# Kernel tuning notes

Hardware: AMD Instinct MI355X
Metric: run time of the kernel (lower is better)

## Reference

```python
import jax, jax.numpy as jnp
import numpy as np

D_MODEL = 512
D_INNER = 1024   # expand * d_model
NH = 16          # heads (headdim 64)
HD = 64
NS = 16          # d_state
HID = 1024       # ff hidden = expand * d_model


def _ln(x, w, b, eps=1e-5):
    m = x.mean(-1, keepdims=True)
    v = ((x - m) ** 2).mean(-1, keepdims=True)
    return (x - m) * jax.lax.rsqrt(v + eps) * w + b


def _rms(x, w, eps=1e-5):
    return x * jax.lax.rsqrt((x * x).mean(-1, keepdims=True) + eps) * w


def _tree_scan(dt, xh, Bv, Cv, pidx, A):
    # dt:[B,T,W,H] xh:[B,T,W,H,P] Bv,Cv:[B,T,W,N] pidx:[B,T,W] A:[H]
    B_, T, W, H = dt.shape
    P = xh.shape[-1]
    N = Bv.shape[-1]
    h0 = jnp.zeros((B_, W, H, P, N), dt.dtype)
    xs = (jnp.moveaxis(dt, 1, 0), jnp.moveaxis(xh, 1, 0),
          jnp.moveaxis(Bv, 1, 0), jnp.moveaxis(Cv, 1, 0),
          jnp.moveaxis(pidx, 1, 0))

    def step(h, inp):
        dt_t, xh_t, b_t, c_t, p_t = inp
        # gather parent state from previous level along the width axis
        hp = jnp.take_along_axis(h, p_t[:, :, None, None, None], axis=1)  # [B,W,H,P,N]
        dA = jnp.exp(dt_t * A)                                            # [B,W,H]
        h_new = dA[..., None, None] * hp \
              + dt_t[..., None, None] * xh_t[..., None] * b_t[:, :, None, None, :]
        y_t = jnp.einsum('bwhpn,bwn->bwhp', h_new, c_t)
        return h_new, y_t

    _, ys = jax.lax.scan(step, h0, xs)
    return jnp.moveaxis(ys, 0, 1)  # [B,T,W,H,P]


def setup_inputs() -> dict:
    key = jax.random.key(0)
    ks = jax.random.split(key, 12)
    B, T, W = 8, 64, 16
    d_in_proj = 2 * D_INNER + 2 * NS + NH  # z | x | B | C | dt
    inp = {
        'x': jax.random.normal(ks[0], (B, T, W, D_MODEL), jnp.float32),
        'parent_pos': jax.random.randint(ks[1], (B, T, W), 0, W, dtype=jnp.int32),
        'ln1_w': jnp.ones((D_MODEL,), jnp.float32),
        'ln1_b': jnp.zeros((D_MODEL,), jnp.float32),
        'in_w': jax.random.normal(ks[2], (D_MODEL, d_in_proj), jnp.float32) * 0.02,
        'in_b': jnp.zeros((d_in_proj,), jnp.float32),
        'A_log': jnp.log(jax.random.uniform(ks[3], (NH,), jnp.float32, 1.0, 16.0)),
        'dt_bias': jnp.full((NH,), -4.0, jnp.float32),
        'Dp': jnp.ones((NH,), jnp.float32),
        'norm_w': jnp.ones((D_INNER,), jnp.float32),
        'out_w': jax.random.normal(ks[4], (D_INNER, D_MODEL), jnp.float32) * 0.02,
        'out_b': jnp.zeros((D_MODEL,), jnp.float32),
        'ln2_w': jnp.ones((D_MODEL,), jnp.float32),
        'ln2_b': jnp.zeros((D_MODEL,), jnp.float32),
        'ff1_w': jax.random.normal(ks[5], (D_MODEL, 2 * HID), jnp.float32) * 0.02,
        'ff1_b': jnp.zeros((2 * HID,), jnp.float32),
        'ff2_w': jax.random.normal(ks[6], (HID, D_MODEL), jnp.float32) * 0.02,
        'ff2_b': jnp.zeros((D_MODEL,), jnp.float32),
    }
    return inp


def reference(x, parent_pos, ln1_w, ln1_b, in_w, in_b, A_log, dt_bias, Dp,
              norm_w, out_w, out_b, ln2_w, ln2_b, ff1_w, ff1_b, ff2_w, ff2_b):
    # norm1 + TreeMamba2 + residual
    xn = _ln(x, ln1_w, ln1_b)
    proj = xn @ in_w + in_b
    z, xp, Bv, Cv, dtr = jnp.split(
        proj, [D_INNER, 2 * D_INNER, 2 * D_INNER + NS, 2 * D_INNER + 2 * NS], axis=-1)
    dt = jax.nn.softplus(dtr + dt_bias)            # [B,T,W,NH]
    A = -jnp.exp(A_log)                            # [NH]
    xh = xp.reshape(*xp.shape[:-1], NH, HD)        # [B,T,W,NH,HD]
    y = _tree_scan(dt, xh, Bv, Cv, parent_pos, A)  # [B,T,W,NH,HD]
    y = y + Dp[..., None] * xh                     # skip connection D*x
    y = y.reshape(*y.shape[:-2], D_INNER)
    y = _rms(y * jax.nn.silu(z), norm_w)           # gated RMSNorm
    y = y @ out_w + out_b
    x = y + x
    # norm2 + gated FF + residual
    yn = _ln(x, ln2_w, ln2_b)
    f = yn @ ff1_w + ff1_b
    f1, g = jnp.split(f, 2, axis=-1)
    f = (f1 * jax.nn.silu(g)) @ ff2_w + ff2_b
    return x + f
```

## Files before the change

### kernel.cpp

```cpp
#include <hip/hip_runtime.h>
#include <hip/hip_bf16.h>
#include <cmath>

#define D_MODEL 512
#define D_INNER 1024
#define NHEAD 16
#define HDIM 64
#define NSTATE 16
#define NB 8
#define NT 64
#define NW 16
#define MROWS 8192
#define PROJ_LD 2176
#define NPROJ 2096

typedef __attribute__((ext_vector_type(8))) short short8;
typedef __attribute__((ext_vector_type(4))) float f32x4;
typedef __hip_bfloat16 bf16;
typedef unsigned int u32;

__device__ __forceinline__ u32 fbits(float f) { return __float_as_uint(f); }
__device__ __forceinline__ float ubits(u32 u) { return __uint_as_float(u); }
__device__ __forceinline__ u32 pack_bf(float a, float b) {
  return (fbits(b) & 0xffff0000u) | (fbits(a) >> 16);
}

template<int N> __device__ __forceinline__ void vmwait() {
  if constexpr (N == 0)      asm volatile("s_waitcnt vmcnt(0)" ::: "memory");
  else if constexpr (N == 2) asm volatile("s_waitcnt vmcnt(2)" ::: "memory");
  else if constexpr (N == 3) asm volatile("s_waitcnt vmcnt(3)" ::: "memory");
  else if constexpr (N == 4) asm volatile("s_waitcnt vmcnt(4)" ::: "memory");
  else if constexpr (N == 6) asm volatile("s_waitcnt vmcnt(6)" ::: "memory");
  else if constexpr (N == 8) asm volatile("s_waitcnt vmcnt(8)" ::: "memory");
  else static_assert(N == 0, "unsupported vmcnt");
}

__device__ __forceinline__ float block_sum(float v, float* sbuf) {
#pragma unroll
  for (int o = 32; o > 0; o >>= 1) v += __shfl_down(v, o, 64);
  int lane = threadIdx.x & 63, wid = threadIdx.x >> 6;
  if (lane == 0) sbuf[wid] = v;
  __syncthreads();
  if (threadIdx.x == 0) {
    float t = 0.f;
    for (int i = 0; i < 4; i++) t += sbuf[i];
    sbuf[0] = t;
  }
  __syncthreads();
  return sbuf[0];
}

__global__ __launch_bounds__(256) void ln512_bf16_kernel(
    const float* __restrict__ x, const float* __restrict__ w,
    const float* __restrict__ b, bf16* __restrict__ out) {
  __shared__ float s1[8], s2[8];
  int row = blockIdx.x;
  const float* xr = x + (size_t)row * D_MODEL;
  bf16* outr = out + (size_t)row * D_MODEL;
  int c0 = threadIdx.x, c1 = threadIdx.x + 256;
  float v0 = xr[c0], v1 = xr[c1];
  float s  = block_sum(v0 + v1, s1);
  float ss = block_sum(v0 * v0 + v1 * v1, s2);
  float mean = s * (1.f / 512.f);
  float var  = ss * (1.f / 512.f) - mean * mean;
  float inv  = rsqrtf(var + 1e-5f);
  outr[c0] = __float2bfloat16((v0 - mean) * inv * w[c0] + b[c0]);
  outr[c1] = __float2bfloat16((v1 - mean) * inv * w[c1] + b[c1]);
}

__global__ __launch_bounds__(256) void wconv_all_kernel(
    const float* __restrict__ in_w, bf16* __restrict__ in_wt,
    const float* __restrict__ out_w, bf16* __restrict__ out_wt,
    const float* __restrict__ ff1_w, bf16* __restrict__ ff1_wt,
    const float* __restrict__ ff2_w, bf16* __restrict__ ff2_wt) {
  __shared__ float tile[32][33];
  int id = blockIdx.x;
  const float* w; bf16* wt;
  int K, N, Npad, bx, by;
  if (id < 1088)      { w = in_w;  wt = in_wt;  K = 512;  N = NPROJ; Npad = PROJ_LD; bx = id % 68;  by = id / 68; }
  else if (id < 1600) { int j = id - 1088; w = out_w; wt = out_wt; K = 1024; N = 512;  Npad = 512;  bx = j % 16; by = j / 16; }
  else if (id < 2624) { int j = id - 1600; w = ff1_w; wt = ff1_wt; K = 512;  N = 2048; Npad = 2048; bx = j % 64; by = j / 64; }
  else                { int j = id - 2624; w = ff2_w; wt = ff2_wt; K = 1024; N = 512;  Npad = 512;  bx = j % 16; by = j / 16; }
  int n0 = bx * 32, k0 = by * 32;
  int tx = threadIdx.x & 31, ty = threadIdx.x >> 5;
#pragma unroll
  for (int i = 0; i < 4; i++) {
    int k = k0 + ty + i * 8, n = n0 + tx;
    tile[ty + i * 8][tx] = (k < K && n < N) ? w[(size_t)k * N + n] : 0.f;
  }
  __syncthreads();
#pragma unroll
  for (int i = 0; i < 4; i++) {
    int n = n0 + ty + i * 8, k = k0 + tx;
    if (n < Npad && k < K)
      wt[(size_t)n * K + k] = __float2bfloat16(tile[tx][ty + i * 8]);
  }
}

template<int BM, int BN, int WN, int MR, int NR>
__global__ __launch_bounds__(256) void mfma_gemm_kernel(
    const bf16* __restrict__ A, const bf16* __restrict__ Bt,
    const float* __restrict__ bias, int nbias,
    const float* __restrict__ resid,
    float* __restrict__ C, int ldc, int K) {
  constexpr int ROWS = BM + BN;
  constexpr int ISS  = ROWS / 64;
  __shared__ __align__(16) bf16 sAB[3][ROWS][32];

  int wid = threadIdx.x >> 6, lane = threadIdx.x & 63;
  int row0 = blockIdx.y * BM, col0 = blockIdx.x * BN;
  int wr = (wid / WN) * (MR * 16);
  int wc = (wid % WN) * (NR * 16);
  int lr = lane >> 2;
  int lc = (lane & 3) * 8;

  f32x4 acc[MR][NR];
#pragma unroll
  for (int m = 0; m < MR; m++)
#pragma unroll
    for (int n = 0; n < NR; n++) acc[m][n] = (f32x4){0.f, 0.f, 0.f, 0.f};

  auto stage = [&](int buf, int k0) {
#pragma unroll
    for (int i = 0; i < ISS; i++) {
      int rb = (wid * ISS + i) * 16;
      int r = rb + lr;
      const bf16* src = (r < BM)
          ? A  + (size_t)(row0 + r) * K + k0 + lc
          : Bt + (size_t)(col0 + (r - BM)) * K + k0 + lc;
      __builtin_amdgcn_global_load_lds(
          (const __attribute__((address_space(1))) void*)src,
          (__attribute__((address_space(3))) void*)&sAB[buf][rb][0], 16, 0, 0);
    }
  };

  stage(0, 0);
  stage(1, 32);
  int cur = 0;
  for (int k0 = 0; k0 < K; k0 += 32) {
    if (k0 + 32 < K) vmwait<ISS>(); else vmwait<0>();
    __builtin_amdgcn_s_barrier();
    asm volatile("" ::: "memory");
    if (k0 + 64 < K) stage(cur == 0 ? 2 : cur - 1, k0 + 64);
    short8 a[MR], b[NR];
    int kk = (lane >> 4) * 8;
#pragma unroll
    for (int m = 0; m < MR; m++)
      a[m] = *(const short8*)&sAB[cur][wr + m * 16 + (lane & 15)][kk];
#pragma unroll
    for (int n = 0; n < NR; n++)
      b[n] = *(const short8*)&sAB[cur][BM + wc + n * 16 + (lane & 15)][kk];
#pragma unroll
    for (int m = 0; m < MR; m++)
#pragma unroll
      for (int n = 0; n < NR; n++)
        acc[m][n] = __builtin_amdgcn_mfma_f32_16x16x32_bf16(a[m], b[n], acc[m][n], 0, 0, 0);
    asm volatile("" ::: "memory");
    cur = (cur == 2) ? 0 : cur + 1;
  }

  int crow = row0 + wr + (lane >> 4) * 4;
  int ccol = col0 + wc + (lane & 15);
#pragma unroll
  for (int m = 0; m < MR; m++) {
#pragma unroll
    for (int n = 0; n < NR; n++) {
      int colg = ccol + n * 16;
      float bv = bias ? ((colg < nbias) ? bias[colg] : 0.f) : 0.f;
#pragma unroll
      for (int j = 0; j < 4; j++) {
        int rowg = crow + m * 16 + j;
        float v = acc[m][n][j] + bv;
        if (resid) v += resid[(size_t)rowg * ldc + colg];
        C[(size_t)rowg * ldc + colg] = v;
      }
    }
  }
}

__global__ __launch_bounds__(256) void inproj_gemm_kernel(
    const bf16* __restrict__ A, const bf16* __restrict__ Bt,
    const float* __restrict__ bias,
    bf16* __restrict__ Cb, float* __restrict__ aux, int K) {
  constexpr int BM = 128, ROWS = 256, ISS = 4;
  __shared__ __align__(16) bf16 sAB[3][ROWS][32];

  int wid = threadIdx.x >> 6, lane = threadIdx.x & 63;
  int row0 = blockIdx.y * BM, col0 = blockIdx.x * 128;
  int wr = (wid >> 1) * 64;
  int wc = (wid & 1) * 64;
  int lr = lane >> 2;
  int lc = (lane & 3) * 8;

  f32x4 acc[4][4];
#pragma unroll
  for (int m = 0; m < 4; m++)
#pragma unroll
    for (int n = 0; n < 4; n++) acc[m][n] = (f32x4){0.f, 0.f, 0.f, 0.f};

  auto stage = [&](int buf, int k0) {
#pragma unroll
    for (int i = 0; i < ISS; i++) {
      int rb = (wid * ISS + i) * 16;
      int r = rb + lr;
      const bf16* src = (r < BM)
          ? A  + (size_t)(row0 + r) * K + k0 + lc
          : Bt + (size_t)(col0 + (r - BM)) * K + k0 + lc;
      __builtin_amdgcn_global_load_lds(
          (const __attribute__((address_space(1))) void*)src,
          (__attribute__((address_space(3))) void*)&sAB[buf][rb][0], 16, 0, 0);
    }
  };

  stage(0, 0);
  stage(1, 32);
  int cur = 0;
  for (int k0 = 0; k0 < K; k0 += 32) {
    if (k0 + 32 < K) vmwait<ISS>(); else vmwait<0>();
    __builtin_amdgcn_s_barrier();
    asm volatile("" ::: "memory");
    if (k0 + 64 < K) stage(cur == 0 ? 2 : cur - 1, k0 + 64);
    short8 a[4], b[4];
    int kk = (lane >> 4) * 8;
#pragma unroll
    for (int m = 0; m < 4; m++)
      a[m] = *(const short8*)&sAB[cur][wr + m * 16 + (lane & 15)][kk];
#pragma unroll
    for (int n = 0; n < 4; n++)
      b[n] = *(const short8*)&sAB[cur][BM + wc + n * 16 + (lane & 15)][kk];
#pragma unroll
    for (int m = 0; m < 4; m++)
#pragma unroll
      for (int n = 0; n < 4; n++)
        acc[m][n] = __builtin_amdgcn_mfma_f32_16x16x32_bf16(a[m], b[n], acc[m][n], 0, 0, 0);
    asm volatile("" ::: "memory");
    cur = (cur == 2) ? 0 : cur + 1;
  }

  int crow = row0 + wr + (lane >> 4) * 4;
  int ccol = col0 + wc + (lane & 15);
#pragma unroll
  for (int m = 0; m < 4; m++) {
#pragma unroll
    for (int n = 0; n < 4; n++) {
      int colg = ccol + n * 16;
      float bv = (colg < NPROJ) ? bias[colg] : 0.f;
#pragma unroll
      for (int j = 0; j < 4; j++) {
        int rowg = crow + m * 16 + j;
        float v = acc[m][n][j] + bv;
        Cb[(size_t)rowg * PROJ_LD + colg] = __float2bfloat16(v);
        if (colg >= 2048 && colg < 2112)
          aux[(size_t)rowg * 64 + (colg - 2048)] = v;
      }
    }
  }
}

__global__ __launch_bounds__(256) void ff1_fused_kernel(
    const bf16* __restrict__ A, const bf16* __restrict__ Bt,
    const float* __restrict__ bias, bf16* __restrict__ out, int K) {
  constexpr int BM = 128, ROWS = 384, ISS = 6;
  __shared__ __align__(16) bf16 sAB[3][ROWS][32];

  int wid = threadIdx.x >> 6, lane = threadIdx.x & 63;
  int row0 = blockIdx.y * BM, col0 = blockIdx.x * 128;
  int wr = (wid >> 1) * 64;
  int wc = (wid & 1) * 64;
  int lr = lane >> 2;
  int lc = (lane & 3) * 8;

  f32x4 acc1[4][4], acc2[4][4];
#pragma unroll
  for (int m = 0; m < 4; m++)
#pragma unroll
    for (int n = 0; n < 4; n++) {
      acc1[m][n] = (f32x4){0.f, 0.f, 0.f, 0.f};
      acc2[m][n] = (f32x4){0.f, 0.f, 0.f, 0.f};
    }

  auto stage = [&](int buf, int k0) {
#pragma unroll
    for (int i = 0; i < ISS; i++) {
      int rb = (wid * ISS + i) * 16;
      int r = rb + lr;
      const bf16* src;
      if (r < BM)       src = A  + (size_t)(row0 + r) * K + k0 + lc;
      else if (r < 256) src = Bt + (size_t)(col0 + (r - 128)) * K + k0 + lc;
      else              src = Bt + (size_t)(1024 + col0 + (r - 256)) * K + k0 + lc;
      __builtin_amdgcn_global_load_lds(
          (const __attribute__((address_space(1))) void*)src,
          (__attribute__((address_space(3))) void*)&sAB[buf][rb][0], 16, 0, 0);
    }
  };

  stage(0, 0);
  stage(1, 32);
  int cur = 0;
  for (int k0 = 0; k0 < K; k0 += 32) {
    if (k0 + 32 < K) vmwait<ISS>(); else vmwait<0>();
    __builtin_amdgcn_s_barrier();
    asm volatile("" ::: "memory");
    if (k0 + 64 < K) stage(cur == 0 ? 2 : cur - 1, k0 + 64);
    short8 a[4], b1[4], b2[4];
    int kk = (lane >> 4) * 8;
#pragma unroll
    for (int m = 0; m < 4; m++)
      a[m] = *(const short8*)&sAB[cur][wr + m * 16 + (lane & 15)][kk];
#pragma unroll
    for (int n = 0; n < 4; n++) {
      b1[n] = *(const short8*)&sAB[cur][128 + wc + n * 16 + (lane & 15)][kk];
      b2[n] = *(const short8*)&sAB[cur][256 + wc + n * 16 + (lane & 15)][kk];
    }
#pragma unroll
    for (int m = 0; m < 4; m++)
#pragma unroll
      for (int n = 0; n < 4; n++) {
        acc1[m][n] = __builtin_amdgcn_mfma_f32_16x16x32_bf16(a[m], b1[n], acc1[m][n], 0, 0, 0);
        acc2[m][n] = __builtin_amdgcn_mfma_f32_16x16x32_bf16(a[m], b2[n], acc2[m][n], 0, 0, 0);
      }
    asm volatile("" ::: "memory");
    cur = (cur == 2) ? 0 : cur + 1;
  }

  int crow = row0 + wr + (lane >> 4) * 4;
  int ccol = col0 + wc + (lane & 15);
#pragma unroll
  for (int m = 0; m < 4; m++) {
#pragma unroll
    for (int n = 0; n < 4; n++) {
      int colg = ccol + n * 16;
      float bv1 = bias[colg];
      float bv2 = bias[1024 + colg];
#pragma unroll
      for (int j = 0; j < 4; j++) {
        int rowg = crow + m * 16 + j;
        float f1 = acc1[m][n][j] + bv1;
        float g  = acc2[m][n][j] + bv2;
        float sg = g / (1.f + expf(-g));
        out[(size_t)rowg * 1024 + colg] = __float2bfloat16(f1 * sg);
      }
    }
  }
}

__global__ __launch_bounds__(256) void tree_scan_kernel(
    const bf16* __restrict__ xb, const float* __restrict__ aux,
    const int* __restrict__ parent,
    const float* __restrict__ A_log, const float* __restrict__ dt_bias,
    const float* __restrict__ Dp, bf16* __restrict__ y) {
  const int tid = threadIdx.x;
  const int ps = blockIdx.x & 3;
  const int h  = (blockIdx.x >> 2) & 15;
  const int b  = blockIdx.x >> 6;
  const int wid = tid >> 6;
  const int lane = tid & 63;
  const int w = lane >> 2;
  const int q = lane & 3;
  const int pl = wid * 4 + q;

  __shared__ __align__(16) u32   BCs[8][16][20];
  __shared__ __align__(16) float dAs[16][8];
  __shared__ __align__(16) float dtss[16][8];
  __shared__ __align__(16) int   pars[16][8];

  const float Ah  = -expf(A_log[h]);
  const float dtb = dt_bias[h];
  const float Dh  = Dp[h];
  const int xcol = 1024 + (h << 6) + (ps << 4) + pl;
  const int ycol = (h << 6) + (ps << 4) + pl;

  float hst[16];
#pragma unroll
  for (int n = 0; n < 16; n++) hst[n] = 0.f;

  const int sp_t = (tid >> 1) >> 4, sp_w = (tid >> 1) & 15, sp_h = tid & 1;

  for (int c = 0; c < 8; c++) {
    const int t0 = c * 8;
    __syncthreads();
    float xv[8];
#pragma unroll
    for (int tt = 0; tt < 8; tt++) {
      size_t row = ((size_t)(b * NT + t0 + tt)) * NW + w;
      xv[tt] = __bfloat162float(xb[row * PROJ_LD + xcol]);
    }
    if (tid < 128) {
      int t = tid >> 4, wv = tid & 15;
      size_t row = ((size_t)(b * NT + t0 + t)) * NW + wv;
      float dtr = aux[row * 64 + 32 + h] + dtb;
      float dtv = (dtr > 20.f) ? dtr : log1pf(expf(dtr));
      dtss[wv][t] = dtv;
      dAs[wv][t]  = expf(dtv * Ah);
      pars[wv][t] = parent[row];
    }
    {
      size_t row = ((size_t)(b * NT + t0 + sp_t)) * NW + sp_w;
      const float* src = aux + row * 64 + sp_h * 16;
      float4 v0 = *(const float4*)&src[0];
      float4 v1 = *(const float4*)&src[4];
      float4 v2 = *(const float4*)&src[8];
      float4 v3 = *(const float4*)&src[12];
      uint4 p0 = {pack_bf(v0.x, v0.y), pack_bf(v0.z, v0.w),
                  pack_bf(v1.x, v1.y), pack_bf(v1.z, v1.w)};
      uint4 p1 = {pack_bf(v2.x, v2.y), pack_bf(v2.z, v2.w),
                  pack_bf(v3.x, v3.y), pack_bf(v3.z, v3.w)};
      *(uint4*)&BCs[sp_t][sp_w][sp_h * 8]     = p0;
      *(uint4*)&BCs[sp_t][sp_w][sp_h * 8 + 4] = p1;
    }
    __syncthreads();
    float dAr[8], dtr8[8];
    int parr[8];
    *(float4*)&dAr[0]  = *(const float4*)&dAs[w][0];
    *(float4*)&dAr[4]  = *(const float4*)&dAs[w][4];
    *(float4*)&dtr8[0] = *(const float4*)&dtss[w][0];
    *(float4*)&dtr8[4] = *(const float4*)&dtss[w][4];
    *(int4*)&parr[0]   = *(const int4*)&pars[w][0];
    *(int4*)&parr[4]   = *(const int4*)&pars[w][4];

#pragma unroll
    for (int tt = 0; tt < 8; tt++) {
      float dA  = dAr[tt];
      float dtx = dtr8[tt] * xv[tt];
      int   par = parr[tt];
      int gidx = (((par << 2) | q) << 2);
      u32 pk[8];
#pragma unroll
      for (int i = 0; i < 8; i++)
        pk[i] = (u32)__builtin_amdgcn_ds_bpermute(
            gidx, (int)pack_bf(hst[2 * i], hst[2 * i + 1]));
      uint4 bA = *(const uint4*)&BCs[tt][w][0];
      uint4 bB = *(const uint4*)&BCs[tt][w][4];
      uint4 cA = *(const uint4*)&BCs[tt][w][8];
      uint4 cB = *(const uint4*)&BCs[tt][w][12];
      u32 bwv[8] = {bA.x, bA.y, bA.z, bA.w, bB.x, bB.y, bB.z, bB.w};
      u32 cwv[8] = {cA.x, cA.y, cA.z, cA.w, cB.x, cB.y, cB.z, cB.w};
      float yv = 0.f;
#pragma unroll
      for (int i = 0; i < 8; i++) {
        u32 g = pk[i], bu = bwv[i], cu = cwv[i];
        float hp0 = ubits(g << 16),  float_hp1_dummy;
        (void)float_hp1_dummy;
        float hp1 = ubits(g & 0xffff0000u);
        float bl  = ubits(bu << 16), bh  = ubits(bu & 0xffff0000u);
        float cl  = ubits(cu << 16), ch  = ubits(cu & 0xffff0000u);
        float h0 = fmaf(dA, hp0, dtx * bl);
        float h1 = fmaf(dA, hp1, dtx * bh);
        hst[2 * i] = h0;
        hst[2 * i + 1] = h1;
        yv = fmaf(h0, cl, fmaf(h1, ch, yv));
      }
      size_t row = ((size_t)(b * NT + t0 + tt)) * NW + w;
      y[row * D_INNER + ycol] = __float2bfloat16(fmaf(Dh, xv[tt], yv));
    }
  }
}

__global__ __launch_bounds__(256) void gate_rms_kernel(
    const bf16* __restrict__ yin, const bf16* __restrict__ projb,
    const float* __restrict__ norm_w, bf16* __restrict__ out) {
  __shared__ float sbuf[8];
  int row = blockIdx.x;
  const bf16* yr = yin + (size_t)row * D_INNER;
  const bf16* zr = projb + (size_t)row * PROJ_LD;
  int c = threadIdx.x * 4;
  bf16 y4[4], z4[4];
  *(uint2*)y4 = *(const uint2*)&yr[c];
  *(uint2*)z4 = *(const uint2*)&zr[c];
  float gv[4];
  float ss = 0.f;
#pragma unroll
  for (int j = 0; j < 4; j++) {
    float z = __bfloat162float(z4[j]);
    float t = __bfloat162float(y4[j]) * (z / (1.f + expf(-z)));
    gv[j] = t;
    ss += t * t;
  }
  ss = block_sum(ss, sbuf);
  float scale = rsqrtf(ss * (1.f / 1024.f) + 1e-5f);
  bf16 o4[4];
#pragma unroll
  for (int j = 0; j < 4; j++) o4[j] = __float2bfloat16(gv[j] * scale * norm_w[c + j]);
  *(uint2*)&out[(size_t)row * D_INNER + c] = *(uint2*)o4;
}

extern "C" void kernel_launch(void* const* d_in, const int* in_sizes, int n_in,
                              void* d_out, int out_size, void* d_ws, size_t ws_size,
                              hipStream_t stream) {
  const float* x       = (const float*)d_in[0];
  const int*   parent  = (const int*)d_in[1];
  const float* ln1_w   = (const float*)d_in[2];
  const float* ln1_b   = (const float*)d_in[3];
  const float* in_w    = (const float*)d_in[4];
  const float* in_b    = (const float*)d_in[5];
  const float* A_log   = (const float*)d_in[6];
  const float* dt_bias = (const float*)d_in[7];
  const float* Dp      = (const float*)d_in[8];
  const float* norm_w  = (const float*)d_in[9];
  const float* out_w   = (const float*)d_in[10];
  const float* out_b   = (const float*)d_in[11];
  const float* ln2_w   = (const float*)d_in[12];
  const float* ln2_b   = (const float*)d_in[13];
  const float* ff1_w   = (const float*)d_in[14];
  const float* ff1_b   = (const float*)d_in[15];
  const float* ff2_w   = (const float*)d_in[16];
  const float* ff2_b   = (const float*)d_in[17];
  float* outp = (float*)d_out;

  char* wp = (char*)d_ws;
  bf16* xnb    = (bf16*)wp;  wp += (size_t)MROWS * D_MODEL * 2;
  bf16* in_wt  = (bf16*)wp;  wp += (size_t)PROJ_LD * D_MODEL * 2;
  bf16* out_wt = (bf16*)wp;  wp += (size_t)D_MODEL * D_INNER * 2;
  bf16* ff1_wt = (bf16*)wp;  wp += (size_t)2048 * D_MODEL * 2;
  bf16* ff2_wt = (bf16*)wp;  wp += (size_t)D_MODEL * D_INNER * 2;
  bf16* projb  = (bf16*)wp;  wp += (size_t)MROWS * PROJ_LD * 2;
  float* aux   = (float*)wp; wp += (size_t)MROWS * 64 * 4;
  bf16* yb     = (bf16*)wp;  wp += (size_t)MROWS * D_INNER * 2;
  bf16* ygb    = (bf16*)wp;  wp += (size_t)MROWS * D_INNER * 2;
  float* xmid  = outp;

  dim3 blk(256);
  wconv_all_kernel<<<3136, blk, 0, stream>>>(
      in_w, in_wt, out_w, out_wt, ff1_w, ff1_wt, ff2_w, ff2_wt);
  ln512_bf16_kernel<<<MROWS, blk, 0, stream>>>(x, ln1_w, ln1_b, xnb);
  inproj_gemm_kernel<<<dim3(PROJ_LD / 128, MROWS / 128), blk, 0, stream>>>(
      xnb, in_wt, in_b, projb, aux, D_MODEL);
  tree_scan_kernel<<<NB * NHEAD * 4, blk, 0, stream>>>(projb, aux, parent,
                                                       A_log, dt_bias, Dp, yb);
  gate_rms_kernel<<<MROWS, blk, 0, stream>>>(yb, projb, norm_w, ygb);
  mfma_gemm_kernel<64, 128, 4, 4, 2><<<dim3(D_MODEL / 128, MROWS / 64), blk, 0, stream>>>(
      ygb, out_wt, out_b, D_MODEL, x, xmid, D_MODEL, D_INNER);
  ln512_bf16_kernel<<<MROWS, blk, 0, stream>>>(xmid, ln2_w, ln2_b, xnb);
  ff1_fused_kernel<<<dim3(8, MROWS / 128), blk, 0, stream>>>(
      xnb, ff1_wt, ff1_b, yb, D_MODEL);
  mfma_gemm_kernel<64, 128, 4, 4, 2><<<dim3(D_MODEL / 128, MROWS / 64), blk, 0, stream>>>(
      yb, ff2_wt, ff2_b, D_MODEL, xmid, outp, D_MODEL, D_INNER);
}
```

Measured before the change: 206.6 us.

## Store scan x in scan-friendly layout and prefetch next chunk's inputs in tree scan

The in-projection GEMM epilogue now splits its output into a separate z buffer and an x buffer laid out by (batch, head, p-slice, t, w, p). This makes the tree-scan's per-timestep x loads contiguous instead of strided rows of width 2176. The tree scan also software-pipelines its global loads: x, B/C, dt and parent for chunk c+1 are issued before computing chunk c, to hide latency. The scattered epilogue stores in the GEMM may be less coalesced, and the prefetch adds register pressure.

```diff
diff --git a/kernel.cpp b/kernel.cpp
--- a/kernel.cpp
+++ b/kernel.cpp
@@ -11,13 +11,13 @@
 #define NT 64
 #define NW 16
 #define MROWS 8192
-#define PROJ_LD 2176
 #define NPROJ 2096
 
 typedef __attribute__((ext_vector_type(8))) short short8;
 typedef __attribute__((ext_vector_type(4))) float f32x4;
 typedef __hip_bfloat16 bf16;
 typedef unsigned int u32;
+typedef unsigned short u16;
 
 __device__ __forceinline__ u32 fbits(float f) { return __float_as_uint(f); }
 __device__ __forceinline__ float ubits(u32 u) { return __uint_as_float(u); }
@@ -77,7 +77,7 @@
   int id = blockIdx.x;
   const float* w; bf16* wt;
   int K, N, Npad, bx, by;
-  if (id < 1088)      { w = in_w;  wt = in_wt;  K = 512;  N = NPROJ; Npad = PROJ_LD; bx = id % 68;  by = id / 68; }
+  if (id < 1088)      { w = in_w;  wt = in_wt;  K = 512;  N = NPROJ; Npad = 2176; bx = id % 68;  by = id / 68; }
   else if (id < 1600) { int j = id - 1088; w = out_w; wt = out_wt; K = 1024; N = 512;  Npad = 512;  bx = j % 16; by = j / 16; }
   else if (id < 2624) { int j = id - 1600; w = ff1_w; wt = ff1_wt; K = 512;  N = 2048; Npad = 2048; bx = j % 64; by = j / 64; }
   else                { int j = id - 2624; w = ff2_w; wt = ff2_wt; K = 1024; N = 512;  Npad = 512;  bx = j % 16; by = j / 16; }
@@ -181,7 +181,8 @@
 __global__ __launch_bounds__(256) void inproj_gemm_kernel(
     const bf16* __restrict__ A, const bf16* __restrict__ Bt,
     const float* __restrict__ bias,
-    bf16* __restrict__ Cb, float* __restrict__ aux, int K) {
+    bf16* __restrict__ zb, bf16* __restrict__ xsc,
+    float* __restrict__ aux, int K) {
   constexpr int BM = 128, ROWS = 256, ISS = 4;
   __shared__ __align__(16) bf16 sAB[3][ROWS][32];
 
@@ -249,9 +250,18 @@
       for (int j = 0; j < 4; j++) {
         int rowg = crow + m * 16 + j;
         float v = acc[m][n][j] + bv;
-        Cb[(size_t)rowg * PROJ_LD + colg] = __float2bfloat16(v);
-        if (colg >= 2048 && colg < 2112)
+        if (colg < 1024) {
+          zb[(size_t)rowg * 1024 + colg] = __float2bfloat16(v);
+        } else if (colg < 2048) {
+          int cx = colg - 1024;
+          int h = cx >> 6, p = cx & 63;
+          int bb = rowg >> 10, t = (rowg >> 4) & 63, w = rowg & 15;
+          size_t idx = ((((size_t)bb * 16 + h) * 4 + (p >> 4)) * 64 + t) * 256
+                     + w * 16 + (p & 15);
+          xsc[idx] = __float2bfloat16(v);
+        } else if (colg < 2112) {
           aux[(size_t)rowg * 64 + (colg - 2048)] = v;
+        }
       }
     }
   }
@@ -345,7 +355,7 @@
 }
 
 __global__ __launch_bounds__(256) void tree_scan_kernel(
-    const bf16* __restrict__ xb, const float* __restrict__ aux,
+    const bf16* __restrict__ xsc, const float* __restrict__ aux,
     const int* __restrict__ parent,
     const float* __restrict__ A_log, const float* __restrict__ dt_bias,
     const float* __restrict__ Dp, bf16* __restrict__ y) {
@@ -367,44 +377,58 @@
   const float Ah  = -expf(A_log[h]);
   const float dtb = dt_bias[h];
   const float Dh  = Dp[h];
-  const int xcol = 1024 + (h << 6) + (ps << 4) + pl;
+  const u16* xp = (const u16*)xsc
+      + ((((size_t)b * 16 + h) * 4 + ps) * 64) * 256 + w * 16 + pl;
   const int ycol = (h << 6) + (ps << 4) + pl;
 
   float hst[16];
 #pragma unroll
   for (int n = 0; n < 16; n++) hst[n] = 0.f;
 
-  const int sp_t = (tid >> 1) >> 4, sp_w = (tid >> 1) & 15, sp_h = tid & 1;
-
+  const int sp_t = tid >> 5, sp_w = (tid >> 1) & 15, sp_h = tid & 1;
+  const int dt_t = tid >> 4, dt_w = tid & 15;
+
+  u16 xpre[8];
+  float4 bc0, bc1, bc2, bc3;
+  float dtpre = 0.f;
+  int papre = 0;
+
+  auto issue = [&](int c) {
+    const int t0 = c * 8;
+#pragma unroll
+    for (int tt = 0; tt < 8; tt++) xpre[tt] = xp[(size_t)(t0 + tt) * 256];
+    size_t row = ((size_t)(b * NT + t0 + sp_t)) * NW + sp_w;
+    const float* src = aux + row * 64 + sp_h * 16;
+    bc0 = *(const float4*)&src[0];
+    bc1 = *(const float4*)&src[4];
+    bc2 = *(const float4*)&src[8];
+    bc3 = *(const float4*)&src[12];
+    if (tid < 128) {
+      size_t r2 = ((size_t)(b * NT + t0 + dt_t)) * NW + dt_w;
+      dtpre = aux[r2 * 64 + 32 + h];
+      papre = parent[r2];
+    }
+  };
+
+  issue(0);
   for (int c = 0; c < 8; c++) {
     const int t0 = c * 8;
     __syncthreads();
     float xv[8];
 #pragma unroll
-    for (int tt = 0; tt < 8; tt++) {
-      size_t row = ((size_t)(b * NT + t0 + tt)) * NW + w;
-      xv[tt] = __bfloat162float(xb[row * PROJ_LD + xcol]);
-    }
+    for (int tt = 0; tt < 8; tt++) xv[tt] = ubits((u32)xpre[tt] << 16);
     if (tid < 128) {
-      int t = tid >> 4, wv = tid & 15;
-      size_t row = ((size_t)(b * NT + t0 + t)) * NW + wv;
-      float dtr = aux[row * 64 + 32 + h] + dtb;
+      float dtr = dtpre + dtb;
       float dtv = (dtr > 20.f) ? dtr : log1pf(expf(dtr));
-      dtss[wv][t] = dtv;
-      dAs[wv][t]  = expf(dtv * Ah);
-      pars[wv][t] = parent[row];
+      dtss[dt_w][dt_t] = dtv;
+      dAs[dt_w][dt_t]  = expf(dtv * Ah);
+      pars[dt_w][dt_t] = papre;
     }
     {
-      size_t row = ((size_t)(b * NT + t0 + sp_t)) * NW + sp_w;
-      const float* src = aux + row * 64 + sp_h * 16;
-      float4 v0 = *(const float4*)&src[0];
-      float4 v1 = *(const float4*)&src[4];
-      float4 v2 = *(const float4*)&src[8];
-      float4 v3 = *(const float4*)&src[12];
-      uint4 p0 = {pack_bf(v0.x, v0.y), pack_bf(v0.z, v0.w),
-                  pack_bf(v1.x, v1.y), pack_bf(v1.z, v1.w)};
-      uint4 p1 = {pack_bf(v2.x, v2.y), pack_bf(v2.z, v2.w),
-                  pack_bf(v3.x, v3.y), pack_bf(v3.z, v3.w)};
+      uint4 p0 = {pack_bf(bc0.x, bc0.y), pack_bf(bc0.z, bc0.w),
+                  pack_bf(bc1.x, bc1.y), pack_bf(bc1.z, bc1.w)};
+      uint4 p1 = {pack_bf(bc2.x, bc2.y), pack_bf(bc2.z, bc2.w),
+                  pack_bf(bc3.x, bc3.y), pack_bf(bc3.z, bc3.w)};
       *(uint4*)&BCs[sp_t][sp_w][sp_h * 8]     = p0;
       *(uint4*)&BCs[sp_t][sp_w][sp_h * 8 + 4] = p1;
     }
@@ -417,6 +441,7 @@
     *(float4*)&dtr8[4] = *(const float4*)&dtss[w][4];
     *(int4*)&parr[0]   = *(const int4*)&pars[w][0];
     *(int4*)&parr[4]   = *(const int4*)&pars[w][4];
+    if (c < 7) issue(c + 1);
 
 #pragma unroll
     for (int tt = 0; tt < 8; tt++) {
@@ -439,8 +464,7 @@
 #pragma unroll
       for (int i = 0; i < 8; i++) {
         u32 g = pk[i], bu = bwv[i], cu = cwv[i];
-        float hp0 = ubits(g << 16),  float_hp1_dummy;
-        (void)float_hp1_dummy;
+        float hp0 = ubits(g << 16);
         float hp1 = ubits(g & 0xffff0000u);
         float bl  = ubits(bu << 16), bh  = ubits(bu & 0xffff0000u);
         float cl  = ubits(cu << 16), ch  = ubits(cu & 0xffff0000u);
@@ -457,12 +481,12 @@
 }
 
 __global__ __launch_bounds__(256) void gate_rms_kernel(
-    const bf16* __restrict__ yin, const bf16* __restrict__ projb,
+    const bf16* __restrict__ yin, const bf16* __restrict__ zb,
     const float* __restrict__ norm_w, bf16* __restrict__ out) {
   __shared__ float sbuf[8];
   int row = blockIdx.x;
   const bf16* yr = yin + (size_t)row * D_INNER;
-  const bf16* zr = projb + (size_t)row * PROJ_LD;
+  const bf16* zr = zb + (size_t)row * D_INNER;
   int c = threadIdx.x * 4;
   bf16 y4[4], z4[4];
   *(uint2*)y4 = *(const uint2*)&yr[c];
@@ -509,11 +533,12 @@
 
   char* wp = (char*)d_ws;
   bf16* xnb    = (bf16*)wp;  wp += (size_t)MROWS * D_MODEL * 2;
-  bf16* in_wt  = (bf16*)wp;  wp += (size_t)PROJ_LD * D_MODEL * 2;
+  bf16* in_wt  = (bf16*)wp;  wp += (size_t)2176 * D_MODEL * 2;
   bf16* out_wt = (bf16*)wp;  wp += (size_t)D_MODEL * D_INNER * 2;
   bf16* ff1_wt = (bf16*)wp;  wp += (size_t)2048 * D_MODEL * 2;
   bf16* ff2_wt = (bf16*)wp;  wp += (size_t)D_MODEL * D_INNER * 2;
-  bf16* projb  = (bf16*)wp;  wp += (size_t)MROWS * PROJ_LD * 2;
+  bf16* zb     = (bf16*)wp;  wp += (size_t)MROWS * D_INNER * 2;
+  bf16* xsc    = (bf16*)wp;  wp += (size_t)MROWS * D_INNER * 2;
   float* aux   = (float*)wp; wp += (size_t)MROWS * 64 * 4;
   bf16* yb     = (bf16*)wp;  wp += (size_t)MROWS * D_INNER * 2;
   bf16* ygb    = (bf16*)wp;  wp += (size_t)MROWS * D_INNER * 2;
@@ -523,11 +548,11 @@
   wconv_all_kernel<<<3136, blk, 0, stream>>>(
       in_w, in_wt, out_w, out_wt, ff1_w, ff1_wt, ff2_w, ff2_wt);
   ln512_bf16_kernel<<<MROWS, blk, 0, stream>>>(x, ln1_w, ln1_b, xnb);
-  inproj_gemm_kernel<<<dim3(PROJ_LD / 128, MROWS / 128), blk, 0, stream>>>(
-      xnb, in_wt, in_b, projb, aux, D_MODEL);
-  tree_scan_kernel<<<NB * NHEAD * 4, blk, 0, stream>>>(projb, aux, parent,
+  inproj_gemm_kernel<<<dim3(2176 / 128, MROWS / 128), blk, 0, stream>>>(
+      xnb, in_wt, in_b, zb, xsc, aux, D_MODEL);
+  tree_scan_kernel<<<NB * NHEAD * 4, blk, 0, stream>>>(xsc, aux, parent,
                                                        A_log, dt_bias, Dp, yb);
-  gate_rms_kernel<<<MROWS, blk, 0, stream>>>(yb, projb, norm_w, ygb);
+  gate_rms_kernel<<<MROWS, blk, 0, stream>>>(yb, zb, norm_w, ygb);
   mfma_gemm_kernel<64, 128, 4, 4, 2><<<dim3(D_MODEL / 128, MROWS / 64), blk, 0, stream>>>(
       ygb, out_wt, out_b, D_MODEL, x, xmid, D_MODEL, D_INNER);
   ln512_bf16_kernel<<<MROWS, blk, 0, stream>>>(xmid, ln2_w, ln2_b, xnb);
```

Result: no change. 204.9 us (-0.8%).
